# Optimization experiments

Measured on AMD Instinct MI355X. Metric: run time of the kernel, lower is better.

The kernel has to match this reference:

```python
import jax, jax.numpy as jnp
import numpy as np

B, T, D, E, K = 2, 2048, 1024, 8, 2
H = 2 * D  # expert hidden

def setup_inputs() -> dict:
    key = jax.random.key(0)
    ks = jax.random.split(key, 5)
    s = 0.02
    return {
        "x": jax.random.normal(ks[0], (B, T, D), jnp.float32),
        "Wr": jax.random.normal(ks[1], (D, E), jnp.float32) * s,
        "br": jnp.zeros((E,), jnp.float32),
        "W1": jax.random.normal(ks[2], (E, D, H), jnp.float32) * s,
        "b1": jnp.zeros((E, H), jnp.float32),
        "W2": jax.random.normal(ks[3], (E, H, D), jnp.float32) * s,
        "b2": jnp.zeros((E, D), jnp.float32),
    }

def reference(x, Wr, br, W1, b1, W2, b2):
    # Router: logits -> top-k -> sparse softmax gates (non-top-k get 0 weight)
    logits = jnp.einsum('btd,de->bte', x, Wr) + br            # [B,T,E]
    topv, topi = jax.lax.top_k(logits, K)                      # [B,T,K]
    sel_mask = (jax.nn.one_hot(topi, E, dtype=logits.dtype).sum(-2) > 0)  # [B,T,E]
    neg_inf = jnp.finfo(logits.dtype).min
    gates = jax.nn.softmax(jnp.where(sel_mask, logits, neg_inf), axis=-1)  # [B,T,E], zero off top-k
    # Experts: final = sum_e gate[...,e] * Expert_e(x). Gate is exactly 0 for
    # non-selected experts, so dense-per-expert compute gives identical math to
    # the gather/scatter loop in the torch module. Dropout is identity (eval).
    h = jax.nn.relu(jnp.einsum('btd,edh->bteh', x, W1) + b1)   # [B,T,E,H]
    out = jnp.einsum('bte,bteh,ehd->btd', gates, h, W2)
    out = out + jnp.einsum('bte,ed->btd', gates, b2)
    return out
```

## Files before the change

kernel.cpp:

```cpp
#include <hip/hip_runtime.h>
#include <hip/hip_bf16.h>
#include <math.h>

namespace {

constexpr int NTOK   = 4096;
constexpr int DDIM   = 1024;
constexpr int E      = 8;
constexpr int HDIM   = 2048;
constexpr int MAXROWS = 8192;
constexpr int MAXBLK  = 72;

typedef __bf16 bf16;
typedef __attribute__((ext_vector_type(4))) __bf16 bf16x4;
typedef __attribute__((ext_vector_type(8))) __bf16 bf16x8;
typedef __attribute__((ext_vector_type(4))) float floatx4;
typedef __attribute__((ext_vector_type(4))) int   i32x4;

__device__ inline void gload_lds16(const bf16* g, bf16* l) {
  __builtin_amdgcn_global_load_lds(
      (const __attribute__((address_space(1))) void*)g,
      (__attribute__((address_space(3))) void*)l, 16, 0, 0);
}

__device__ inline bf16x8 ds_read16(const bf16* p) {
  i32x4 r;
  asm volatile("ds_read_b128 %0, %1"
               : "=v"(r)
               : "v"((const __attribute__((address_space(3))) bf16*)p));
  return __builtin_bit_cast(bf16x8, r);
}

__global__ void init_kernel(int* counts) {
  counts[threadIdx.x] = 0;
}

__global__ void router_kernel(const float* __restrict__ x,
                              const float* __restrict__ Wr,
                              const float* __restrict__ br,
                              int* __restrict__ counts,
                              int* __restrict__ topk_e,
                              float* __restrict__ topk_g,
                              bf16* __restrict__ xb) {
  int wave = threadIdx.x >> 6;
  int lane = threadIdx.x & 63;
  int t0 = (blockIdx.x * 4 + wave) * 2;

  float acc[16];
#pragma unroll
  for (int j = 0; j < 16; ++j) acc[j] = 0.f;

#pragma unroll
  for (int i = 0; i < DDIM / 64; ++i) {
    int d = i * 64 + lane;
    float4 w0 = *(const float4*)(Wr + (size_t)d * E);
    float4 w1 = *(const float4*)(Wr + (size_t)d * E + 4);
#pragma unroll
    for (int t = 0; t < 2; ++t) {
      float xv = x[(size_t)(t0 + t) * DDIM + d];
      xb[(size_t)(t0 + t) * DDIM + d] = (bf16)xv;
      acc[t * 8 + 0] += xv * w0.x; acc[t * 8 + 1] += xv * w0.y;
      acc[t * 8 + 2] += xv * w0.z; acc[t * 8 + 3] += xv * w0.w;
      acc[t * 8 + 4] += xv * w1.x; acc[t * 8 + 5] += xv * w1.y;
      acc[t * 8 + 6] += xv * w1.z; acc[t * 8 + 7] += xv * w1.w;
    }
  }
#pragma unroll
  for (int off = 32; off > 0; off >>= 1) {
#pragma unroll
    for (int j = 0; j < 16; ++j) acc[j] += __shfl_xor(acc[j], off, 64);
  }
  if (lane == 0) {
#pragma unroll
    for (int t = 0; t < 2; ++t) {
      int tt = t0 + t;
      float lg[E];
#pragma unroll
      for (int e = 0; e < E; ++e) lg[e] = acc[t * 8 + e] + br[e];
      int e0 = 0;
#pragma unroll
      for (int e = 1; e < E; ++e) if (lg[e] > lg[e0]) e0 = e;
      int e1 = (e0 == 0) ? 1 : 0;
#pragma unroll
      for (int e = 0; e < E; ++e) if (e != e0 && lg[e] > lg[e1]) e1 = e;
      float ex = expf(lg[e1] - lg[e0]);
      float s = 1.f + ex;
      topk_e[2 * tt]     = e0;
      topk_e[2 * tt + 1] = e1;
      topk_g[2 * tt]     = 1.f / s;
      topk_g[2 * tt + 1] = ex / s;
      atomicAdd(&counts[e0 * 16], 1);
      atomicAdd(&counts[e1 * 16], 1);
    }
  }
}

__global__ void scan_kernel(const int* __restrict__ counts,
                            int* __restrict__ offsets,
                            int* __restrict__ cursor,
                            int* __restrict__ blockmap,
                            int* __restrict__ nblk) {
  if (threadIdx.x == 0 && blockIdx.x == 0) {
    int s = 0, nb = 0;
    for (int e = 0; e < E; ++e) {
      offsets[e] = s; cursor[e * 16] = s;
      int c = counts[e * 16];
      int nt = (c + 127) >> 7;
      for (int m = 0; m < nt; ++m) blockmap[nb++] = (e << 16) | m;
      s += c;
    }
    offsets[E] = s;
    nblk[0] = nb;
  }
}

__global__ void scatter_kernel(const int* __restrict__ topk_e,
                               int* __restrict__ cursor,
                               int* __restrict__ rowtok,
                               int* __restrict__ tokrow) {
  int t = blockIdx.x * 256 + threadIdx.x;
  int lane = threadIdx.x & 63;
  unsigned long long lt = ((unsigned long long)1 << lane) - 1;
#pragma unroll
  for (int k = 0; k < 2; ++k) {
    int e = topk_e[2 * t + k];
#pragma unroll
    for (int ee = 0; ee < E; ++ee) {
      unsigned long long m = __ballot(e == ee);
      if (m) {
        int leader = __ffsll((long long)m) - 1;
        int base = 0;
        if (lane == leader) base = atomicAdd(&cursor[ee * 16], __popcll(m));
        base = __shfl(base, leader, 64);
        if (e == ee) {
          int row = base + __popcll(m & lt);
          rowtok[row] = t;
          tokrow[2 * t + k] = row;
        }
      }
    }
  }
}

__global__ void transpose_cast_kernel(const float* __restrict__ in, bf16* __restrict__ out,
                                      int R, int C) {
  __shared__ bf16 tile[64][72];
  const float* src = in + (size_t)blockIdx.z * R * C;
  bf16* dst = out + (size_t)blockIdx.z * R * C;
  int c0 = blockIdx.x * 64, r0 = blockIdx.y * 64;
  int tr = threadIdx.x >> 4;
  int tc = (threadIdx.x & 15) * 4;
#pragma unroll
  for (int i = 0; i < 4; ++i) {
    int r = tr + i * 16;
    float4 v = *(const float4*)(src + (size_t)(r0 + r) * C + c0 + tc);
    bf16x4 o;
    o[0] = (bf16)v.x; o[1] = (bf16)v.y; o[2] = (bf16)v.z; o[3] = (bf16)v.w;
    *(bf16x4*)&tile[r][tc] = o;
  }
  __syncthreads();
  int tr2 = threadIdx.x >> 3;
  int tc2 = (threadIdx.x & 7) * 8;
#pragma unroll
  for (int i = 0; i < 2; ++i) {
    int c = tr2 + i * 32;
    bf16x8 v;
#pragma unroll
    for (int j = 0; j < 8; ++j) v[j] = tile[tc2 + j][c];
    *(bf16x8*)(dst + (size_t)(c0 + c) * R + r0 + tc2) = v;
  }
}

template <bool GATHER, bool RELU>
__global__ __launch_bounds__(256) void ffn_gemm(
    const bf16* __restrict__ A, const bf16* __restrict__ W,
    const float* __restrict__ bias, bf16* __restrict__ Y,
    const int* __restrict__ rowtok, const int* __restrict__ offsets,
    const int* __restrict__ counts,
    const int* __restrict__ blockmap, const int* __restrict__ nblk,
    int Kdim, int Ndim) {
  static_assert(MAXBLK == 72, "XCD remap assumes gridDim.x == 72 == 8*9");
  int xcd = blockIdx.x & 7;
  int idx = blockIdx.y * (MAXBLK / 8) + (blockIdx.x >> 3);
  int mIdx = idx % MAXBLK;
  int nIdx = xcd + 8 * (idx / MAXBLK);
  if (mIdx >= nblk[0]) return;
  int bm = blockmap[mIdx];
  int e = bm >> 16;
  int mBase = (bm & 0xffff) << 7;
  int cnt = counts[e * 16];
  int rowBase = offsets[e] + mBase;
  int nBase = nIdx * 128;
  int validRows = cnt - mBase; if (validRows > 128) validRows = 128;

  __shared__ bf16 Asm[2][128 * 64];
  __shared__ bf16 Bsm[2][128 * 64];

  int tid = threadIdx.x;
  int wave = tid >> 6, lane = tid & 63;
  int lrow = lane >> 3;
  int lseg = lane & 7;
  int sseg = lseg ^ lrow;

  const bf16* aptr[4];
  const bf16* bptr[4];
#pragma unroll
  for (int i = 0; i < 4; ++i) {
    int c = wave + i * 4;
    int r = rowBase + c * 8 + lrow;
    if (r > MAXROWS - 1) r = MAXROWS - 1;
    size_t rowoff = GATHER ? (size_t)rowtok[r] * Kdim : (size_t)r * Kdim;
    aptr[i] = A + rowoff + sseg * 8;
    bptr[i] = W + ((size_t)e * Ndim + nBase + c * 8 + lrow) * (size_t)Kdim + sseg * 8;
  }

  floatx4 acc[4][4];
#pragma unroll
  for (int m = 0; m < 4; ++m)
#pragma unroll
    for (int n = 0; n < 4; ++n) acc[m][n] = floatx4{0.f, 0.f, 0.f, 0.f};

  int wm = wave & 1, wn = wave >> 1;
  int mrow = lane & 15;
  int kseg0 = lane >> 4;
  int swz = mrow & 7;

  auto issue = [&](int p, int kc) {
#pragma unroll
    for (int i = 0; i < 4; ++i) {
      int c = wave + i * 4;
      gload_lds16(aptr[i] + kc, &Asm[p][c * 512]);
      gload_lds16(bptr[i] + kc, &Bsm[p][c * 512]);
    }
  };

  issue(0, 0);
  int p = 0;
  for (int kc = 0; kc < Kdim; kc += 64) {
    if (kc + 64 < Kdim) {
      issue(p ^ 1, kc + 64);
      asm volatile("s_waitcnt vmcnt(8)" ::: "memory");
    } else {
      asm volatile("s_waitcnt vmcnt(0)" ::: "memory");
    }
    asm volatile("s_barrier" ::: "memory");

    bf16x8 af[2][4], bfr[2][4];
#pragma unroll
    for (int ks = 0; ks < 2; ++ks) {
      int kk = (((ks << 2) | kseg0) ^ swz) << 3;
#pragma unroll
      for (int m = 0; m < 4; ++m)
        af[ks][m] = ds_read16(&Asm[p][(wm * 64 + m * 16 + mrow) * 64 + kk]);
#pragma unroll
      for (int n = 0; n < 4; ++n)
        bfr[ks][n] = ds_read16(&Bsm[p][(wn * 64 + n * 16 + mrow) * 64 + kk]);
    }
    asm volatile("s_waitcnt lgkmcnt(0)" ::: "memory");
    __builtin_amdgcn_sched_barrier(0);

#pragma unroll
    for (int ks = 0; ks < 2; ++ks)
#pragma unroll
      for (int m = 0; m < 4; ++m)
#pragma unroll
        for (int n = 0; n < 4; ++n)
          acc[m][n] = __builtin_amdgcn_mfma_f32_16x16x32_bf16(af[ks][m], bfr[ks][n], acc[m][n], 0, 0, 0);

    asm volatile("s_barrier" ::: "memory");
    p ^= 1;
  }

  int crow = (lane >> 4) * 4;
  int ccol = lane & 15;
#pragma unroll
  for (int n = 0; n < 4; ++n) {
    int colg = nBase + wn * 64 + n * 16 + ccol;
    float bv = bias[(size_t)e * Ndim + colg];
#pragma unroll
    for (int m = 0; m < 4; ++m) {
#pragma unroll
      for (int r = 0; r < 4; ++r) {
        int rl = wm * 64 + m * 16 + crow + r;
        if (rl < validRows) {
          float v = acc[m][n][r] + bv;
          if (RELU) v = fmaxf(v, 0.f);
          Y[(size_t)(rowBase + rl) * Ndim + colg] = (bf16)v;
        }
      }
    }
  }
}

__global__ void combine_kernel(const bf16* __restrict__ Y2,
                               const int* __restrict__ tokrow,
                               const float* __restrict__ topk_g,
                               float* __restrict__ out) {
  int idx = blockIdx.x * 256 + threadIdx.x;
  int t = idx >> 7;
  int d8 = (idx & 127) * 8;
  int r0 = tokrow[2 * t], r1 = tokrow[2 * t + 1];
  float g0 = topk_g[2 * t], g1 = topk_g[2 * t + 1];
  bf16x8 a = *(const bf16x8*)(Y2 + (size_t)r0 * DDIM + d8);
  bf16x8 b = *(const bf16x8*)(Y2 + (size_t)r1 * DDIM + d8);
  float o[8];
#pragma unroll
  for (int j = 0; j < 8; ++j) o[j] = g0 * (float)a[j] + g1 * (float)b[j];
  float* op = out + (size_t)t * DDIM + d8;
  *(float4*)op = *(float4*)&o[0];
  *(float4*)(op + 4) = *(float4*)&o[4];
}

}

extern "C" void kernel_launch(void* const* d_in, const int* in_sizes, int n_in,
                              void* d_out, int out_size, void* d_ws, size_t ws_size,
                              hipStream_t stream) {
  const float* x  = (const float*)d_in[0];
  const float* Wr = (const float*)d_in[1];
  const float* br = (const float*)d_in[2];
  const float* W1 = (const float*)d_in[3];
  const float* b1 = (const float*)d_in[4];
  const float* W2 = (const float*)d_in[5];
  const float* b2 = (const float*)d_in[6];
  float* out = (float*)d_out;

  char* w = (char*)d_ws;
  int*   counts   = (int*)(w);
  int*   cursor   = (int*)(w + 512);
  int*   offsets  = (int*)(w + 1024);
  int*   blockmap = (int*)(w + 2048);
  int*   nblk     = (int*)(w + 2048 + 512);
  int*   topk_e   = (int*)(w + 4096);
  float* topk_g   = (float*)(w + 4096 + 32768);
  int*   rowtok   = (int*)(w + 4096 + 65536);
  int*   tokrow   = (int*)(w + 4096 + 98304);
  char*  big      = w + 4096 + 131072;
  bf16* xb  = (bf16*)(big);
  bf16* W1T = (bf16*)(big + 8388608);
  bf16* W2T = (bf16*)(big + 8388608 + 33554432);
  bf16* Y1  = (bf16*)(big + 8388608 + 67108864);
  bf16* Y2  = (bf16*)(big + 8388608);

  init_kernel<<<1, 128, 0, stream>>>(counts);
  transpose_cast_kernel<<<dim3(HDIM / 64, DDIM / 64, E), 256, 0, stream>>>(W1, W1T, DDIM, HDIM);
  transpose_cast_kernel<<<dim3(DDIM / 64, HDIM / 64, E), 256, 0, stream>>>(W2, W2T, HDIM, DDIM);
  router_kernel<<<NTOK / 8, 256, 0, stream>>>(x, Wr, br, counts, topk_e, topk_g, xb);
  scan_kernel<<<1, 1, 0, stream>>>(counts, offsets, cursor, blockmap, nblk);
  scatter_kernel<<<NTOK / 256, 256, 0, stream>>>(topk_e, cursor, rowtok, tokrow);
  ffn_gemm<true, true><<<dim3(MAXBLK, HDIM / 128), 256, 0, stream>>>(
      xb, W1T, b1, Y1, rowtok, offsets, counts, blockmap, nblk, DDIM, HDIM);
  ffn_gemm<false, false><<<dim3(MAXBLK, DDIM / 128), 256, 0, stream>>>(
      Y1, W2T, b2, Y2, rowtok, offsets, counts, blockmap, nblk, HDIM, DDIM);
  combine_kernel<<<NTOK * DDIM / 8 / 256, 256, 0, stream>>>(Y2, tokrow, topk_g, out);
}
```

Baseline: 376.7 us.

## Use 256x256 tiles with 8-wave ping-pong pipeline in expert GEMMs

After: 398.6 us. 1.06x slower.

```diff
diff --git a/kernel.cpp b/kernel.cpp
--- a/kernel.cpp
+++ b/kernel.cpp
@@ -9,7 +9,7 @@
 constexpr int E      = 8;
 constexpr int HDIM   = 2048;
 constexpr int MAXROWS = 8192;
-constexpr int MAXBLK  = 72;
+constexpr int MAXMB   = 40;
 
 typedef __bf16 bf16;
 typedef __attribute__((ext_vector_type(4))) __bf16 bf16x4;
@@ -105,7 +105,7 @@
     for (int e = 0; e < E; ++e) {
       offsets[e] = s; cursor[e * 16] = s;
       int c = counts[e * 16];
-      int nt = (c + 127) >> 7;
+      int nt = (c + 255) >> 8;
       for (int m = 0; m < nt; ++m) blockmap[nb++] = (e << 16) | m;
       s += c;
     }
@@ -172,116 +172,172 @@
 }
 
 template <bool GATHER, bool RELU>
-__global__ __launch_bounds__(256) void ffn_gemm(
+__global__ __launch_bounds__(512, 2) void ffn_gemm(
     const bf16* __restrict__ A, const bf16* __restrict__ W,
     const float* __restrict__ bias, bf16* __restrict__ Y,
     const int* __restrict__ rowtok, const int* __restrict__ offsets,
     const int* __restrict__ counts,
     const int* __restrict__ blockmap, const int* __restrict__ nblk,
     int Kdim, int Ndim) {
-  static_assert(MAXBLK == 72, "XCD remap assumes gridDim.x == 72 == 8*9");
+  int NY  = Ndim >> 8;
   int xcd = blockIdx.x & 7;
-  int idx = blockIdx.y * (MAXBLK / 8) + (blockIdx.x >> 3);
-  int mIdx = idx % MAXBLK;
-  int nIdx = xcd + 8 * (idx / MAXBLK);
+  int local = blockIdx.y * (MAXMB / 8) + (blockIdx.x >> 3);
+  int gpx = 8 / NY;
+  int nIdx = xcd / gpx;
+  int mIdx = (xcd % gpx) * (MAXMB / gpx) + local;
   if (mIdx >= nblk[0]) return;
   int bm = blockmap[mIdx];
   int e = bm >> 16;
-  int mBase = (bm & 0xffff) << 7;
+  int mBase = (bm & 0xffff) << 8;
   int cnt = counts[e * 16];
   int rowBase = offsets[e] + mBase;
-  int nBase = nIdx * 128;
-  int validRows = cnt - mBase; if (validRows > 128) validRows = 128;
-
-  __shared__ bf16 Asm[2][128 * 64];
-  __shared__ bf16 Bsm[2][128 * 64];
+  int nBase = nIdx << 8;
+  int validRows = cnt - mBase; if (validRows > 256) validRows = 256;
+
+  __shared__ bf16 Asm[2][2][256][32];
+  __shared__ bf16 Bsm[2][2][256][32];
 
   int tid = threadIdx.x;
   int wave = tid >> 6, lane = tid & 63;
-  int lrow = lane >> 3;
-  int lseg = lane & 7;
-  int sseg = lseg ^ lrow;
-
-  const bf16* aptr[4];
-  const bf16* bptr[4];
-#pragma unroll
-  for (int i = 0; i < 4; ++i) {
-    int c = wave + i * 4;
-    int r = rowBase + c * 8 + lrow;
-    if (r > MAXROWS - 1) r = MAXROWS - 1;
-    size_t rowoff = GATHER ? (size_t)rowtok[r] * Kdim : (size_t)r * Kdim;
-    aptr[i] = A + rowoff + sseg * 8;
-    bptr[i] = W + ((size_t)e * Ndim + nBase + c * 8 + lrow) * (size_t)Kdim + sseg * 8;
-  }
-
-  floatx4 acc[4][4];
-#pragma unroll
-  for (int m = 0; m < 4; ++m)
+
+  int srow = tid >> 2;
+  int sseg = tid & 3;
+  int swz  = sseg ^ (srow & 3);
+
+  const bf16 *aR0, *aR1, *bR0, *bR1;
+  {
+    int r0 = rowBase + srow, r1 = rowBase + srow + 128;
+    if (r0 > MAXROWS - 1) r0 = MAXROWS - 1;
+    if (r1 > MAXROWS - 1) r1 = MAXROWS - 1;
+    size_t ro0 = GATHER ? (size_t)rowtok[r0] * Kdim : (size_t)r0 * Kdim;
+    size_t ro1 = GATHER ? (size_t)rowtok[r1] * Kdim : (size_t)r1 * Kdim;
+    aR0 = A + ro0 + swz * 8;
+    aR1 = A + ro1 + swz * 8;
+    size_t wb = (size_t)e * Ndim;
+    bR0 = W + (wb + nBase + srow) * (size_t)Kdim + swz * 8;
+    bR1 = W + (wb + nBase + srow + 128) * (size_t)Kdim + swz * 8;
+  }
+
+  auto stageA = [&](int d, int kh, int kb) {
+    bf16* l = &Asm[d][kh][0][0] + wave * 512;
+    gload_lds16(aR0 + kb, l);
+    gload_lds16(aR1 + kb, l + 4096);
+  };
+  auto stageB = [&](int d, int kh, int kb) {
+    bf16* l = &Bsm[d][kh][0][0] + wave * 512;
+    gload_lds16(bR0 + kb, l);
+    gload_lds16(bR1 + kb, l + 4096);
+  };
+
+  int wm2 = wave >> 2;
+  int wn2 = wave & 3;
+  int frow = lane & 15;
+  int rseg = (((lane >> 4) ^ (lane & 3)) << 3);
+
+  floatx4 acc[8][4];
+#pragma unroll
+  for (int m = 0; m < 8; ++m)
 #pragma unroll
     for (int n = 0; n < 4; ++n) acc[m][n] = floatx4{0.f, 0.f, 0.f, 0.f};
 
-  int wm = wave & 1, wn = wave >> 1;
-  int mrow = lane & 15;
-  int kseg0 = lane >> 4;
-  int swz = mrow & 7;
-
-  auto issue = [&](int p, int kc) {
-#pragma unroll
-    for (int i = 0; i < 4; ++i) {
-      int c = wave + i * 4;
-      gload_lds16(aptr[i] + kc, &Asm[p][c * 512]);
-      gload_lds16(bptr[i] + kc, &Bsm[p][c * 512]);
-    }
-  };
-
-  issue(0, 0);
-  int p = 0;
-  for (int kc = 0; kc < Kdim; kc += 64) {
-    if (kc + 64 < Kdim) {
-      issue(p ^ 1, kc + 64);
-      asm volatile("s_waitcnt vmcnt(8)" ::: "memory");
-    } else {
-      asm volatile("s_waitcnt vmcnt(0)" ::: "memory");
-    }
-    asm volatile("s_barrier" ::: "memory");
-
-    bf16x8 af[2][4], bfr[2][4];
-#pragma unroll
-    for (int ks = 0; ks < 2; ++ks) {
-      int kk = (((ks << 2) | kseg0) ^ swz) << 3;
-#pragma unroll
-      for (int m = 0; m < 4; ++m)
-        af[ks][m] = ds_read16(&Asm[p][(wm * 64 + m * 16 + mrow) * 64 + kk]);
-#pragma unroll
-      for (int n = 0; n < 4; ++n)
-        bfr[ks][n] = ds_read16(&Bsm[p][(wn * 64 + n * 16 + mrow) * 64 + kk]);
-    }
+  int nkt = Kdim >> 6;
+
+  stageA(0, 0, 0); stageB(0, 0, 0); stageA(0, 1, 32); stageB(0, 1, 32);
+  asm volatile("s_waitcnt vmcnt(4)" ::: "memory");
+  asm volatile("s_barrier" ::: "memory");
+
+  bf16x8 af[4], bfr[4];
+  int d = 0;
+  for (int kt = 0; kt < nkt; ++kt) {
+    bool more = (kt + 1 < nkt);
+    int kb = (kt + 1) << 6;
+
+#pragma unroll
+    for (int n = 0; n < 4; ++n)
+      bfr[n] = ds_read16(&Bsm[d][0][wn2 * 64 + n * 16 + frow][0] + rseg);
+#pragma unroll
+    for (int m = 0; m < 4; ++m)
+      af[m] = ds_read16(&Asm[d][0][wm2 * 128 + m * 16 + frow][0] + rseg);
+    if (more) stageA(d ^ 1, 0, kb);
+    asm volatile("s_barrier" ::: "memory");
     asm volatile("s_waitcnt lgkmcnt(0)" ::: "memory");
     __builtin_amdgcn_sched_barrier(0);
-
-#pragma unroll
-    for (int ks = 0; ks < 2; ++ks)
-#pragma unroll
-      for (int m = 0; m < 4; ++m)
-#pragma unroll
-        for (int n = 0; n < 4; ++n)
-          acc[m][n] = __builtin_amdgcn_mfma_f32_16x16x32_bf16(af[ks][m], bfr[ks][n], acc[m][n], 0, 0, 0);
-
-    asm volatile("s_barrier" ::: "memory");
-    p ^= 1;
+    __builtin_amdgcn_s_setprio(1);
+#pragma unroll
+    for (int m = 0; m < 4; ++m)
+#pragma unroll
+      for (int n = 0; n < 4; ++n)
+        acc[m][n] = __builtin_amdgcn_mfma_f32_16x16x32_bf16(af[m], bfr[n], acc[m][n], 0, 0, 0);
+    __builtin_amdgcn_s_setprio(0);
+    asm volatile("s_barrier" ::: "memory");
+
+#pragma unroll
+    for (int m = 0; m < 4; ++m)
+      af[m] = ds_read16(&Asm[d][0][wm2 * 128 + (m + 4) * 16 + frow][0] + rseg);
+    if (more) stageB(d ^ 1, 0, kb);
+    asm volatile("s_barrier" ::: "memory");
+    asm volatile("s_waitcnt lgkmcnt(0)" ::: "memory");
+    __builtin_amdgcn_sched_barrier(0);
+    __builtin_amdgcn_s_setprio(1);
+#pragma unroll
+    for (int m = 0; m < 4; ++m)
+#pragma unroll
+      for (int n = 0; n < 4; ++n)
+        acc[m + 4][n] = __builtin_amdgcn_mfma_f32_16x16x32_bf16(af[m], bfr[n], acc[m + 4][n], 0, 0, 0);
+    __builtin_amdgcn_s_setprio(0);
+    if (more) asm volatile("s_waitcnt vmcnt(4)" ::: "memory");
+    else      asm volatile("s_waitcnt vmcnt(0)" ::: "memory");
+    asm volatile("s_barrier" ::: "memory");
+
+#pragma unroll
+    for (int n = 0; n < 4; ++n)
+      bfr[n] = ds_read16(&Bsm[d][1][wn2 * 64 + n * 16 + frow][0] + rseg);
+#pragma unroll
+    for (int m = 0; m < 4; ++m)
+      af[m] = ds_read16(&Asm[d][1][wm2 * 128 + m * 16 + frow][0] + rseg);
+    if (more) stageA(d ^ 1, 1, kb + 32);
+    asm volatile("s_barrier" ::: "memory");
+    asm volatile("s_waitcnt lgkmcnt(0)" ::: "memory");
+    __builtin_amdgcn_sched_barrier(0);
+    __builtin_amdgcn_s_setprio(1);
+#pragma unroll
+    for (int m = 0; m < 4; ++m)
+#pragma unroll
+      for (int n = 0; n < 4; ++n)
+        acc[m][n] = __builtin_amdgcn_mfma_f32_16x16x32_bf16(af[m], bfr[n], acc[m][n], 0, 0, 0);
+    __builtin_amdgcn_s_setprio(0);
+    asm volatile("s_barrier" ::: "memory");
+
+#pragma unroll
+    for (int m = 0; m < 4; ++m)
+      af[m] = ds_read16(&Asm[d][1][wm2 * 128 + (m + 4) * 16 + frow][0] + rseg);
+    if (more) stageB(d ^ 1, 1, kb + 32);
+    asm volatile("s_barrier" ::: "memory");
+    asm volatile("s_waitcnt lgkmcnt(0)" ::: "memory");
+    __builtin_amdgcn_sched_barrier(0);
+    __builtin_amdgcn_s_setprio(1);
+#pragma unroll
+    for (int m = 0; m < 4; ++m)
+#pragma unroll
+      for (int n = 0; n < 4; ++n)
+        acc[m + 4][n] = __builtin_amdgcn_mfma_f32_16x16x32_bf16(af[m], bfr[n], acc[m + 4][n], 0, 0, 0);
+    __builtin_amdgcn_s_setprio(0);
+    if (more) asm volatile("s_waitcnt vmcnt(4)" ::: "memory");
+    asm volatile("s_barrier" ::: "memory");
+    d ^= 1;
   }
 
   int crow = (lane >> 4) * 4;
   int ccol = lane & 15;
 #pragma unroll
   for (int n = 0; n < 4; ++n) {
-    int colg = nBase + wn * 64 + n * 16 + ccol;
+    int colg = nBase + wn2 * 64 + n * 16 + ccol;
     float bv = bias[(size_t)e * Ndim + colg];
 #pragma unroll
-    for (int m = 0; m < 4; ++m) {
+    for (int m = 0; m < 8; ++m) {
 #pragma unroll
       for (int r = 0; r < 4; ++r) {
-        int rl = wm * 64 + m * 16 + crow + r;
+        int rl = wm2 * 128 + m * 16 + crow + r;
         if (rl < validRows) {
           float v = acc[m][n][r] + bv;
           if (RELU) v = fmaxf(v, 0.f);
@@ -348,9 +404,9 @@
   router_kernel<<<NTOK / 8, 256, 0, stream>>>(x, Wr, br, counts, topk_e, topk_g, xb);
   scan_kernel<<<1, 1, 0, stream>>>(counts, offsets, cursor, blockmap, nblk);
   scatter_kernel<<<NTOK / 256, 256, 0, stream>>>(topk_e, cursor, rowtok, tokrow);
-  ffn_gemm<true, true><<<dim3(MAXBLK, HDIM / 128), 256, 0, stream>>>(
+  ffn_gemm<true, true><<<dim3(MAXMB, HDIM / 256), 512, 0, stream>>>(
       xb, W1T, b1, Y1, rowtok, offsets, counts, blockmap, nblk, DDIM, HDIM);
-  ffn_gemm<false, false><<<dim3(MAXBLK, DDIM / 128), 256, 0, stream>>>(
+  ffn_gemm<false, false><<<dim3(MAXMB, DDIM / 256), 512, 0, stream>>>(
       Y1, W2T, b2, Y2, rowtok, offsets, counts, blockmap, nblk, HDIM, DDIM);
   combine_kernel<<<NTOK * DDIM / 8 / 256, 256, 0, stream>>>(Y2, tokrow, topk_g, out);
 }
```

## Switch expert GEMM to triple-buffered BK=32 pipeline with one barrier per step

Applied to the files above, without the earlier changes.

Result: no change. 377.5 us (+0.2%).

```diff
diff --git a/kernel.cpp b/kernel.cpp
--- a/kernel.cpp
+++ b/kernel.cpp
@@ -172,14 +172,13 @@
 }
 
 template <bool GATHER, bool RELU>
-__global__ __launch_bounds__(256) void ffn_gemm(
+__global__ __launch_bounds__(256, 3) void ffn_gemm(
     const bf16* __restrict__ A, const bf16* __restrict__ W,
     const float* __restrict__ bias, bf16* __restrict__ Y,
     const int* __restrict__ rowtok, const int* __restrict__ offsets,
     const int* __restrict__ counts,
     const int* __restrict__ blockmap, const int* __restrict__ nblk,
     int Kdim, int Ndim) {
-  static_assert(MAXBLK == 72, "XCD remap assumes gridDim.x == 72 == 8*9");
   int xcd = blockIdx.x & 7;
   int idx = blockIdx.y * (MAXBLK / 8) + (blockIdx.x >> 3);
   int mIdx = idx % MAXBLK;
@@ -193,26 +192,38 @@
   int nBase = nIdx * 128;
   int validRows = cnt - mBase; if (validRows > 128) validRows = 128;
 
-  __shared__ bf16 Asm[2][128 * 64];
-  __shared__ bf16 Bsm[2][128 * 64];
+  __shared__ bf16 Asm[3][128][32];
+  __shared__ bf16 Bsm[3][128][32];
 
   int tid = threadIdx.x;
   int wave = tid >> 6, lane = tid & 63;
-  int lrow = lane >> 3;
-  int lseg = lane & 7;
-  int sseg = lseg ^ lrow;
-
-  const bf16* aptr[4];
-  const bf16* bptr[4];
-#pragma unroll
-  for (int i = 0; i < 4; ++i) {
-    int c = wave + i * 4;
-    int r = rowBase + c * 8 + lrow;
-    if (r > MAXROWS - 1) r = MAXROWS - 1;
-    size_t rowoff = GATHER ? (size_t)rowtok[r] * Kdim : (size_t)r * Kdim;
-    aptr[i] = A + rowoff + sseg * 8;
-    bptr[i] = W + ((size_t)e * Ndim + nBase + c * 8 + lrow) * (size_t)Kdim + sseg * 8;
-  }
+
+  int soct = (lane & 3) ^ ((lane >> 3) & 3);
+  const bf16 *aP0, *aP1, *bP0, *bP1;
+  {
+    int r0 = rowBase + wave * 32 + (lane >> 2);
+    int r1 = r0 + 16;
+    if (r0 > MAXROWS - 1) r0 = MAXROWS - 1;
+    if (r1 > MAXROWS - 1) r1 = MAXROWS - 1;
+    size_t ro0 = GATHER ? (size_t)rowtok[r0] * Kdim : (size_t)r0 * Kdim;
+    size_t ro1 = GATHER ? (size_t)rowtok[r1] * Kdim : (size_t)r1 * Kdim;
+    aP0 = A + ro0 + soct * 8;
+    aP1 = A + ro1 + soct * 8;
+    size_t wb = ((size_t)e * Ndim + nBase + wave * 32 + (lane >> 2)) * (size_t)Kdim;
+    bP0 = W + wb + soct * 8;
+    bP1 = W + wb + (size_t)16 * Kdim + soct * 8;
+  }
+
+  auto stage = [&](int buf, int kc) {
+    gload_lds16(aP0 + kc, &Asm[buf][wave * 32][0]);
+    gload_lds16(aP1 + kc, &Asm[buf][wave * 32 + 16][0]);
+    gload_lds16(bP0 + kc, &Bsm[buf][wave * 32][0]);
+    gload_lds16(bP1 + kc, &Bsm[buf][wave * 32 + 16][0]);
+  };
+
+  int wm = wave & 1, wn = wave >> 1;
+  int frow = lane & 15;
+  int roff = (((lane >> 4) ^ ((frow >> 1) & 3)) << 3);
 
   floatx4 acc[4][4];
 #pragma unroll
@@ -220,55 +231,36 @@
 #pragma unroll
     for (int n = 0; n < 4; ++n) acc[m][n] = floatx4{0.f, 0.f, 0.f, 0.f};
 
-  int wm = wave & 1, wn = wave >> 1;
-  int mrow = lane & 15;
-  int kseg0 = lane >> 4;
-  int swz = mrow & 7;
-
-  auto issue = [&](int p, int kc) {
-#pragma unroll
-    for (int i = 0; i < 4; ++i) {
-      int c = wave + i * 4;
-      gload_lds16(aptr[i] + kc, &Asm[p][c * 512]);
-      gload_lds16(bptr[i] + kc, &Bsm[p][c * 512]);
-    }
-  };
-
-  issue(0, 0);
-  int p = 0;
-  for (int kc = 0; kc < Kdim; kc += 64) {
-    if (kc + 64 < Kdim) {
-      issue(p ^ 1, kc + 64);
-      asm volatile("s_waitcnt vmcnt(8)" ::: "memory");
-    } else {
-      asm volatile("s_waitcnt vmcnt(0)" ::: "memory");
-    }
+  int nkt = Kdim >> 5;
+
+  stage(0, 0);
+  stage(1, 32);
+  int r = 0;
+  for (int t = 0; t < nkt; ++t) {
+    if (t + 1 < nkt) asm volatile("s_waitcnt vmcnt(4)" ::: "memory");
+    else             asm volatile("s_waitcnt vmcnt(0)" ::: "memory");
     asm volatile("s_barrier" ::: "memory");
-
-    bf16x8 af[2][4], bfr[2][4];
-#pragma unroll
-    for (int ks = 0; ks < 2; ++ks) {
-      int kk = (((ks << 2) | kseg0) ^ swz) << 3;
-#pragma unroll
-      for (int m = 0; m < 4; ++m)
-        af[ks][m] = ds_read16(&Asm[p][(wm * 64 + m * 16 + mrow) * 64 + kk]);
-#pragma unroll
-      for (int n = 0; n < 4; ++n)
-        bfr[ks][n] = ds_read16(&Bsm[p][(wn * 64 + n * 16 + mrow) * 64 + kk]);
-    }
+    if (t + 2 < nkt) {
+      int s = r + 2; if (s >= 3) s -= 3;
+      stage(s, (t + 2) * 32);
+    }
+    bf16x8 af[4], bfr[4];
+#pragma unroll
+    for (int m = 0; m < 4; ++m)
+      af[m] = ds_read16(&Asm[r][wm * 64 + m * 16 + frow][0] + roff);
+#pragma unroll
+    for (int n = 0; n < 4; ++n)
+      bfr[n] = ds_read16(&Bsm[r][wn * 64 + n * 16 + frow][0] + roff);
     asm volatile("s_waitcnt lgkmcnt(0)" ::: "memory");
     __builtin_amdgcn_sched_barrier(0);
-
-#pragma unroll
-    for (int ks = 0; ks < 2; ++ks)
-#pragma unroll
-      for (int m = 0; m < 4; ++m)
-#pragma unroll
-        for (int n = 0; n < 4; ++n)
-          acc[m][n] = __builtin_amdgcn_mfma_f32_16x16x32_bf16(af[ks][m], bfr[ks][n], acc[m][n], 0, 0, 0);
-
-    asm volatile("s_barrier" ::: "memory");
-    p ^= 1;
+    __builtin_amdgcn_s_setprio(1);
+#pragma unroll
+    for (int m = 0; m < 4; ++m)
+#pragma unroll
+      for (int n = 0; n < 4; ++n)
+        acc[m][n] = __builtin_amdgcn_mfma_f32_16x16x32_bf16(af[m], bfr[n], acc[m][n], 0, 0, 0);
+    __builtin_amdgcn_s_setprio(0);
+    ++r; if (r == 3) r = 0;
   }
 
   int crow = (lane >> 4) * 4;
@@ -280,10 +272,10 @@
 #pragma unroll
     for (int m = 0; m < 4; ++m) {
 #pragma unroll
-      for (int r = 0; r < 4; ++r) {
-        int rl = wm * 64 + m * 16 + crow + r;
+      for (int rr = 0; rr < 4; ++rr) {
+        int rl = wm * 64 + m * 16 + crow + rr;
         if (rl < validRows) {
-          float v = acc[m][n][r] + bv;
+          float v = acc[m][n][rr] + bv;
           if (RELU) v = fmaxf(v, 0.f);
           Y[(size_t)(rowBase + rl) * Ndim + colg] = (bf16)v;
         }
```

## Fuse weight transposes with router, merge scan and scatter into one kernel

Applied to the files above, without the earlier changes.

Measured after the change: 403.6 us. +7.1%, slower.

```diff
diff --git a/kernel.cpp b/kernel.cpp
--- a/kernel.cpp
+++ b/kernel.cpp
@@ -31,20 +31,61 @@
   return __builtin_bit_cast(bf16x8, r);
 }
 
-__global__ void init_kernel(int* counts) {
-  counts[threadIdx.x] = 0;
-}
-
-__global__ void router_kernel(const float* __restrict__ x,
-                              const float* __restrict__ Wr,
-                              const float* __restrict__ br,
-                              int* __restrict__ counts,
-                              int* __restrict__ topk_e,
-                              float* __restrict__ topk_g,
-                              bf16* __restrict__ xb) {
+__device__ inline void transpose_tile(const float* __restrict__ src,
+                                      bf16* __restrict__ dst,
+                                      int R, int C, int c0, int r0,
+                                      bf16 (*tile)[66]) {
+  int tid = threadIdx.x;
+  int tr = tid >> 4;
+  int tc = (tid & 15) * 4;
+#pragma unroll
+  for (int i = 0; i < 4; ++i) {
+    int r = tr + i * 16;
+    float4 v = *(const float4*)(src + (size_t)(r0 + r) * C + c0 + tc);
+    bf16x4 o;
+    o[0] = (bf16)v.x; o[1] = (bf16)v.y; o[2] = (bf16)v.z; o[3] = (bf16)v.w;
+    *(bf16x4*)&tile[r][tc] = o;
+  }
+  __syncthreads();
+  int tr2 = tid >> 3;
+  int tc2 = (tid & 7) * 8;
+#pragma unroll
+  for (int i = 0; i < 2; ++i) {
+    int c = tr2 + i * 32;
+    bf16x8 v;
+#pragma unroll
+    for (int j = 0; j < 8; ++j) v[j] = tile[tc2 + j][c];
+    *(bf16x8*)(dst + (size_t)(c0 + c) * R + r0 + tc2) = v;
+  }
+}
+
+__global__ __launch_bounds__(256) void prep_kernel(
+    const float* __restrict__ x,  const float* __restrict__ Wr,
+    const float* __restrict__ br, const float* __restrict__ W1,
+    const float* __restrict__ W2,
+    int* __restrict__ topk_e, float* __restrict__ topk_g,
+    bf16* __restrict__ xb, bf16* __restrict__ W1T, bf16* __restrict__ W2T) {
+  __shared__ bf16 tile[64][66];
+  int b = blockIdx.x;
+  if (b < 4096) {
+    int bx = b & 31, by = (b >> 5) & 15, bz = b >> 9;
+    const float* src = W1 + (size_t)bz * DDIM * HDIM;
+    bf16* dst = W1T + (size_t)bz * DDIM * HDIM;
+    transpose_tile(src, dst, DDIM, HDIM, bx * 64, by * 64, tile);
+    return;
+  }
+  if (b < 8192) {
+    int lb = b - 4096;
+    int bx = lb & 15, by = (lb >> 4) & 31, bz = lb >> 9;
+    const float* src = W2 + (size_t)bz * DDIM * HDIM;
+    bf16* dst = W2T + (size_t)bz * DDIM * HDIM;
+    transpose_tile(src, dst, HDIM, DDIM, bx * 64, by * 64, tile);
+    return;
+  }
+  int rb = b - 8192;
   int wave = threadIdx.x >> 6;
   int lane = threadIdx.x & 63;
-  int t0 = (blockIdx.x * 4 + wave) * 2;
+  int t0 = (rb * 4 + wave) * 2;
 
   float acc[16];
 #pragma unroll
@@ -89,22 +130,38 @@
       topk_e[2 * tt + 1] = e1;
       topk_g[2 * tt]     = 1.f / s;
       topk_g[2 * tt + 1] = ex / s;
-      atomicAdd(&counts[e0 * 16], 1);
-      atomicAdd(&counts[e1 * 16], 1);
-    }
-  }
-}
-
-__global__ void scan_kernel(const int* __restrict__ counts,
-                            int* __restrict__ offsets,
-                            int* __restrict__ cursor,
-                            int* __restrict__ blockmap,
-                            int* __restrict__ nblk) {
-  if (threadIdx.x == 0 && blockIdx.x == 0) {
+    }
+  }
+}
+
+__global__ __launch_bounds__(256) void scan_scatter_kernel(
+    const int* __restrict__ topk_e,
+    int* __restrict__ counts,
+    int* __restrict__ offsets,
+    int* __restrict__ blockmap, int* __restrict__ nblk,
+    int* __restrict__ rowtok, int* __restrict__ tokrow) {
+  __shared__ int hist[E], curs[E];
+  int tid = threadIdx.x;
+  int lane = tid & 63;
+  unsigned long long lt = ((unsigned long long)1 << lane) - 1;
+  if (tid < E) hist[tid] = 0;
+  __syncthreads();
+  for (int i = tid; i < 2 * NTOK; i += 256) {
+    int e = topk_e[i];
+#pragma unroll
+    for (int ee = 0; ee < E; ++ee) {
+      unsigned long long m = __ballot(e == ee);
+      if (m && lane == __ffsll((long long)m) - 1) atomicAdd(&hist[ee], __popcll(m));
+    }
+  }
+  __syncthreads();
+  if (tid == 0) {
     int s = 0, nb = 0;
     for (int e = 0; e < E; ++e) {
-      offsets[e] = s; cursor[e * 16] = s;
-      int c = counts[e * 16];
+      int c = hist[e];
+      curs[e] = s;
+      counts[e * 16] = c;
+      offsets[e] = s;
       int nt = (c + 127) >> 7;
       for (int m = 0; m < nt; ++m) blockmap[nb++] = (e << 16) | m;
       s += c;
@@ -112,62 +169,24 @@
     offsets[E] = s;
     nblk[0] = nb;
   }
-}
-
-__global__ void scatter_kernel(const int* __restrict__ topk_e,
-                               int* __restrict__ cursor,
-                               int* __restrict__ rowtok,
-                               int* __restrict__ tokrow) {
-  int t = blockIdx.x * 256 + threadIdx.x;
-  int lane = threadIdx.x & 63;
-  unsigned long long lt = ((unsigned long long)1 << lane) - 1;
-#pragma unroll
-  for (int k = 0; k < 2; ++k) {
-    int e = topk_e[2 * t + k];
+  __syncthreads();
+  for (int i = tid; i < 2 * NTOK; i += 256) {
+    int e = topk_e[i];
 #pragma unroll
     for (int ee = 0; ee < E; ++ee) {
       unsigned long long m = __ballot(e == ee);
       if (m) {
         int leader = __ffsll((long long)m) - 1;
         int base = 0;
-        if (lane == leader) base = atomicAdd(&cursor[ee * 16], __popcll(m));
+        if (lane == leader) base = atomicAdd(&curs[ee], __popcll(m));
         base = __shfl(base, leader, 64);
         if (e == ee) {
           int row = base + __popcll(m & lt);
-          rowtok[row] = t;
-          tokrow[2 * t + k] = row;
+          rowtok[row] = i >> 1;
+          tokrow[i] = row;
         }
       }
     }
-  }
-}
-
-__global__ void transpose_cast_kernel(const float* __restrict__ in, bf16* __restrict__ out,
-                                      int R, int C) {
-  __shared__ bf16 tile[64][72];
-  const float* src = in + (size_t)blockIdx.z * R * C;
-  bf16* dst = out + (size_t)blockIdx.z * R * C;
-  int c0 = blockIdx.x * 64, r0 = blockIdx.y * 64;
-  int tr = threadIdx.x >> 4;
-  int tc = (threadIdx.x & 15) * 4;
-#pragma unroll
-  for (int i = 0; i < 4; ++i) {
-    int r = tr + i * 16;
-    float4 v = *(const float4*)(src + (size_t)(r0 + r) * C + c0 + tc);
-    bf16x4 o;
-    o[0] = (bf16)v.x; o[1] = (bf16)v.y; o[2] = (bf16)v.z; o[3] = (bf16)v.w;
-    *(bf16x4*)&tile[r][tc] = o;
-  }
-  __syncthreads();
-  int tr2 = threadIdx.x >> 3;
-  int tc2 = (threadIdx.x & 7) * 8;
-#pragma unroll
-  for (int i = 0; i < 2; ++i) {
-    int c = tr2 + i * 32;
-    bf16x8 v;
-#pragma unroll
-    for (int j = 0; j < 8; ++j) v[j] = tile[tc2 + j][c];
-    *(bf16x8*)(dst + (size_t)(c0 + c) * R + r0 + tc2) = v;
   }
 }
 
@@ -327,7 +346,6 @@
 
   char* w = (char*)d_ws;
   int*   counts   = (int*)(w);
-  int*   cursor   = (int*)(w + 512);
   int*   offsets  = (int*)(w + 1024);
   int*   blockmap = (int*)(w + 2048);
   int*   nblk     = (int*)(w + 2048 + 512);
@@ -342,12 +360,9 @@
   bf16* Y1  = (bf16*)(big + 8388608 + 67108864);
   bf16* Y2  = (bf16*)(big + 8388608);
 
-  init_kernel<<<1, 128, 0, stream>>>(counts);
-  transpose_cast_kernel<<<dim3(HDIM / 64, DDIM / 64, E), 256, 0, stream>>>(W1, W1T, DDIM, HDIM);
-  transpose_cast_kernel<<<dim3(DDIM / 64, HDIM / 64, E), 256, 0, stream>>>(W2, W2T, HDIM, DDIM);
-  router_kernel<<<NTOK / 8, 256, 0, stream>>>(x, Wr, br, counts, topk_e, topk_g, xb);
-  scan_kernel<<<1, 1, 0, stream>>>(counts, offsets, cursor, blockmap, nblk);
-  scatter_kernel<<<NTOK / 256, 256, 0, stream>>>(topk_e, cursor, rowtok, tokrow);
+  prep_kernel<<<8704, 256, 0, stream>>>(x, Wr, br, W1, W2, topk_e, topk_g, xb, W1T, W2T);
+  scan_scatter_kernel<<<1, 256, 0, stream>>>(topk_e, counts, offsets, blockmap, nblk,
+                                             rowtok, tokrow);
   ffn_gemm<true, true><<<dim3(MAXBLK, HDIM / 128), 256, 0, stream>>>(
       xb, W1T, b1, Y1, rowtok, offsets, counts, blockmap, nblk, DDIM, HDIM);
   ffn_gemm<false, false><<<dim3(MAXBLK, DDIM / 128), 256, 0, stream>>>(
```
